# Performance work log

Measured on AMD Instinct MI355X. Metric: run time of the kernel, lower is better.

The kernel has to match this reference:

```python
import jax, jax.numpy as jnp
import numpy as np

N, IN_DIM, OUT_DIM = 8192, 512, 256
ALPHA = 0.2
NEG_INF = -9e15


def setup_inputs() -> dict:
    key = jax.random.key(0)
    k1, k2, k3, k4 = jax.random.split(key, 4)
    node_features = jax.random.normal(k1, (N, IN_DIM), dtype=jnp.float32)
    adj_matrix = jax.random.randint(k2, (N, N), 0, 2, dtype=jnp.int32)
    # xavier-uniform linear weight [out,in] -> store as [in,out]
    lim_w = float(np.sqrt(6.0 / (IN_DIM + OUT_DIM)))
    W = jax.random.uniform(k3, (IN_DIM, OUT_DIM), dtype=jnp.float32, minval=-lim_w, maxval=lim_w)
    b = jnp.zeros((OUT_DIM,), dtype=jnp.float32)
    # attention Linear(2*out_dim, 1): weight a [2*out_dim], bias scalar
    lim_a = float(np.sqrt(6.0 / (2 * OUT_DIM + 1)))
    a = jax.random.uniform(k4, (2 * OUT_DIM,), dtype=jnp.float32, minval=-lim_a, maxval=lim_a)
    a_bias = jnp.zeros((), dtype=jnp.float32)
    return {"adj_matrix": adj_matrix, "node_features": node_features, "W": W, "b": b, "a": a, "a_bias": a_bias}


def reference(adj_matrix, node_features, W, b, a, a_bias):
    # h = Linear(node_features); dropout is identity in eval mode
    h = node_features @ W + b                     # [N, D]
    # attention(cat(h_i, h_j)) == h_i @ a_l + h_j @ a_r + a_bias
    a_l, a_r = a[:OUT_DIM], a[OUT_DIM:]
    e_l = h @ a_l                                 # [N]
    e_r = h @ a_r                                 # [N]
    e = jax.nn.leaky_relu(e_l[:, None] + e_r[None, :] + a_bias, ALPHA)  # [N, N]
    scores = jnp.where(adj_matrix > 0, e, NEG_INF)
    attention = jax.nn.softmax(scores, axis=1)    # [N, N]
    h_prime = attention @ h                       # [N, D]
    return h_prime
```

## Files before the change

### kernel.cpp

```cpp
#include <hip/hip_runtime.h>

#define N 8192
#define DIN 512
#define DOUT 256
#define ALPHA 0.2f
#define NEG_INF -9.0e15f

typedef __attribute__((ext_vector_type(8))) short bf16x8;
typedef __attribute__((ext_vector_type(4))) float f32x4;
typedef __attribute__((ext_vector_type(4))) int   i32x4;

__device__ __forceinline__ unsigned f2bf_u(float f) {
    unsigned u = __builtin_bit_cast(unsigned, f);
    return (u + 0x7fffu + ((u >> 16) & 1u)) >> 16;
}
__device__ __forceinline__ unsigned pack2bf(float lo, float hi) {
    return f2bf_u(lo) | (f2bf_u(hi) << 16);
}
union U4BF8 { uint4 u; bf16x8 v; };

__device__ __forceinline__ void async_copy16(const ushort* g, ushort* l) {
    __builtin_amdgcn_global_load_lds(
        (const __attribute__((address_space(1))) unsigned*)g,
        (__attribute__((address_space(3))) unsigned*)l, 16, 0, 0);
}

__global__ __launch_bounds__(256) void wb_kernel(const float* __restrict__ W,
                                                 ushort* __restrict__ WB) {
    const int g = blockIdx.x * 256 + threadIdx.x;
    const int c = g & 255, k8 = g >> 8;
    const float* wp = W + (size_t)(k8 * 8) * DOUT + c;
    U4BF8 o;
    o.u.x = pack2bf(wp[0 * DOUT], wp[1 * DOUT]);
    o.u.y = pack2bf(wp[2 * DOUT], wp[3 * DOUT]);
    o.u.z = pack2bf(wp[4 * DOUT], wp[5 * DOUT]);
    o.u.w = pack2bf(wp[6 * DOUT], wp[7 * DOUT]);
    *(uint4*)(WB + (size_t)g * 8) = o.u;
}

__global__ __launch_bounds__(256) void h_kernel(
        const float* __restrict__ X, const ushort* __restrict__ WB,
        const float* __restrict__ bvec, const float* __restrict__ a,
        ushort* __restrict__ hB, float* __restrict__ el, float* __restrict__ er)
{
    __shared__ float red[4][64][65];
    __shared__ float elr[2][4][16];
    const int t = threadIdx.x;
    const int w = t >> 6, l = t & 63, q = l >> 4, n = l & 15;
    const int i0 = blockIdx.x * 16;
    f32x4 acc[16];
    #pragma unroll
    for (int ct = 0; ct < 16; ++ct) acc[ct] = (f32x4){0.f, 0.f, 0.f, 0.f};
    const float* xp = X + (size_t)(i0 + n) * DIN + q * 8;

    #pragma unroll
    for (int ks = 0; ks < 4; ++ks) {
        const int k0 = w * 128 + ks * 32;
        const float4 x0 = *(const float4*)(xp + k0);
        const float4 x1 = *(const float4*)(xp + k0 + 4);
        U4BF8 pa;
        pa.u.x = pack2bf(x0.x, x0.y); pa.u.y = pack2bf(x0.z, x0.w);
        pa.u.z = pack2bf(x1.x, x1.y); pa.u.w = pack2bf(x1.z, x1.w);
        const ushort* wbp = WB + ((k0 >> 3) + q) * 2048 + n * 8;
        bf16x8 bfr[16];
        #pragma unroll
        for (int ct = 0; ct < 16; ++ct) bfr[ct] = *(const bf16x8*)(wbp + ct * 128);
        #pragma unroll
        for (int ct = 0; ct < 16; ++ct)
            acc[ct] = __builtin_amdgcn_mfma_f32_16x16x32_bf16(pa.v, bfr[ct], acc[ct], 0, 0, 0);
    }
    #pragma unroll
    for (int ct = 0; ct < 16; ++ct)
        #pragma unroll
        for (int r = 0; r < 4; ++r) red[w][l][ct * 4 + r] = acc[ct][r];
    __syncthreads();

    float pl[4] = {0.f, 0.f, 0.f, 0.f}, pr[4] = {0.f, 0.f, 0.f, 0.f};
    const int hbase = (blockIdx.x * 2 + (q >> 1)) * 2048 + n * 8 + (q & 1) * 4;
    #pragma unroll
    for (int c2 = 0; c2 < 4; ++c2) {
        const int ct = w * 4 + c2;
        const float bb = bvec[ct * 16 + n];
        const float al = a[ct * 16 + n];
        const float ar = a[DOUT + ct * 16 + n];
        float v[4];
        #pragma unroll
        for (int r = 0; r < 4; ++r) {
            v[r] = red[0][l][ct * 4 + r] + red[1][l][ct * 4 + r]
                 + red[2][l][ct * 4 + r] + red[3][l][ct * 4 + r] + bb;
            pl[r] += v[r] * al;
            pr[r] += v[r] * ar;
        }
        ushort4 hp;
        hp.x = (ushort)f2bf_u(v[0]); hp.y = (ushort)f2bf_u(v[1]);
        hp.z = (ushort)f2bf_u(v[2]); hp.w = (ushort)f2bf_u(v[3]);
        *(ushort4*)&hB[hbase + ct * 128] = hp;
    }
    #pragma unroll
    for (int r = 0; r < 4; ++r) {
        #pragma unroll
        for (int off = 1; off < 16; off <<= 1) {
            pl[r] += __shfl_xor(pl[r], off);
            pr[r] += __shfl_xor(pr[r], off);
        }
    }
    if (n == 0) {
        #pragma unroll
        for (int r = 0; r < 4; ++r) {
            elr[0][w][q * 4 + r] = pl[r];
            elr[1][w][q * 4 + r] = pr[r];
        }
    }
    __syncthreads();
    if (t < 16) {
        el[i0 + t] = elr[0][0][t] + elr[0][1][t] + elr[0][2][t] + elr[0][3][t];
        er[i0 + t] = elr[1][0][t] + elr[1][1][t] + elr[1][2][t] + elr[1][3][t];
    }
}

__global__ __launch_bounds__(512, 1) void attn_kernel(
        const int* __restrict__ adj, const float* __restrict__ el,
        const float* __restrict__ er, const float* __restrict__ ab,
        const ushort* __restrict__ hB, float* __restrict__ pout,
        float* __restrict__ plsum)
{
    __shared__ ushort stage[2][32768];
    __shared__ float ers[2048];
    const int t = threadIdx.x;
    const int w = t >> 6, l = t & 63, q = l >> 4, n = l & 15;
    const int rb = blockIdx.x >> 2, jq = blockIdx.x & 3;
    const int j0 = jq * 2048;
    const int row = rb * 128 + w * 16 + n;
    const float elm = el[row] + ab[0];
    const int* alp = adj + (size_t)row * N + j0 + q * 8;

    f32x4 acc[16];
    #pragma unroll
    for (int ct = 0; ct < 16; ++ct) acc[ct] = (f32x4){0.f, 0.f, 0.f, 0.f};
    float lsum = 0.f;

    *(float4*)&ers[t * 4] = *(const float4*)&er[j0 + t * 4];
    i32x4 a[8];
    #pragma unroll
    for (int kg = 0; kg < 4; ++kg) {
        a[2 * kg]     = __builtin_nontemporal_load((const i32x4*)(alp + kg * 32));
        a[2 * kg + 1] = __builtin_nontemporal_load((const i32x4*)(alp + kg * 32 + 4));
    }
    {
        const ushort* g = hB + (size_t)j0 * 256 + t * 8;
        ushort* lb = &stage[0][t * 8];
        #pragma unroll
        for (int i = 0; i < 8; ++i) async_copy16(g + i * 4096, lb + i * 4096);
    }

    for (int s = 0; s < 16; ++s) {
        __syncthreads();
        if (s < 15) {
            const ushort* g = hB + (size_t)(j0 + (s + 1) * 128) * 256 + t * 8;
            ushort* lb = &stage[(s + 1) & 1][t * 8];
            #pragma unroll
            for (int i = 0; i < 8; ++i) async_copy16(g + i * 4096, lb + i * 4096);
        }
        U4BF8 pa[4];
        #pragma unroll
        for (int kg = 0; kg < 4; ++kg) {
            const float4 e0 = *(const float4*)&ers[s * 128 + kg * 32 + q * 8];
            const float4 e1 = *(const float4*)&ers[s * 128 + kg * 32 + q * 8 + 4];
            const i32x4 a0 = a[2 * kg], a1 = a[2 * kg + 1];
            float v, p0, p1, p2, p3, p4, p5, p6, p7;
            v = elm + e0.x; v = fmaxf(v, ALPHA * v); p0 = __expf(a0.x > 0 ? v : NEG_INF);
            v = elm + e0.y; v = fmaxf(v, ALPHA * v); p1 = __expf(a0.y > 0 ? v : NEG_INF);
            v = elm + e0.z; v = fmaxf(v, ALPHA * v); p2 = __expf(a0.z > 0 ? v : NEG_INF);
            v = elm + e0.w; v = fmaxf(v, ALPHA * v); p3 = __expf(a0.w > 0 ? v : NEG_INF);
            v = elm + e1.x; v = fmaxf(v, ALPHA * v); p4 = __expf(a1.x > 0 ? v : NEG_INF);
            v = elm + e1.y; v = fmaxf(v, ALPHA * v); p5 = __expf(a1.y > 0 ? v : NEG_INF);
            v = elm + e1.z; v = fmaxf(v, ALPHA * v); p6 = __expf(a1.z > 0 ? v : NEG_INF);
            v = elm + e1.w; v = fmaxf(v, ALPHA * v); p7 = __expf(a1.w > 0 ? v : NEG_INF);
            lsum += p0 + p1 + p2 + p3 + p4 + p5 + p6 + p7;
            pa[kg].u.x = pack2bf(p0, p1); pa[kg].u.y = pack2bf(p2, p3);
            pa[kg].u.z = pack2bf(p4, p5); pa[kg].u.w = pack2bf(p6, p7);
        }
        if (s < 15) {
            const int* ap = alp + (s + 1) * 128;
            #pragma unroll
            for (int kg = 0; kg < 4; ++kg) {
                a[2 * kg]     = __builtin_nontemporal_load((const i32x4*)(ap + kg * 32));
                a[2 * kg + 1] = __builtin_nontemporal_load((const i32x4*)(ap + kg * 32 + 4));
            }
        }
        #pragma unroll
        for (int kg = 0; kg < 4; ++kg) {
            const ushort* sb = &stage[s & 1][(kg * 4 + q) * 2048 + n * 8];
            #pragma unroll
            for (int ct = 0; ct < 16; ++ct) {
                const bf16x8 bf = *(const bf16x8*)(sb + ct * 128);
                acc[ct] = __builtin_amdgcn_mfma_f32_16x16x32_bf16(pa[kg].v, bf, acc[ct], 0, 0, 0);
            }
        }
    }

    lsum += __shfl_xor(lsum, 16);
    lsum += __shfl_xor(lsum, 32);
    if (l < 16) plsum[(size_t)jq * N + row] = lsum;

    float* pb = pout + ((size_t)jq * N + rb * 128 + w * 16 + q * 4) * 256 + n;
    #pragma unroll
    for (int ct = 0; ct < 16; ++ct)
        #pragma unroll
        for (int r = 0; r < 4; ++r)
            __builtin_nontemporal_store(acc[ct][r], pb + (size_t)r * 256 + ct * 16);
}

__global__ __launch_bounds__(256) void combine_kernel(
        const float* __restrict__ pout, const float* __restrict__ plsum,
        float* __restrict__ out)
{
    const int t = threadIdx.x;
    const int row = blockIdx.x * 4 + (t >> 6);
    const int c = (t & 63) * 4;
    const size_t idx = (size_t)row * 256 + c;
    const size_t qs = (size_t)N * 256;
    float4 v0 = *(const float4*)&pout[idx];
    float4 v1 = *(const float4*)&pout[idx + qs];
    float4 v2 = *(const float4*)&pout[idx + 2 * qs];
    float4 v3 = *(const float4*)&pout[idx + 3 * qs];
    const float li = 1.0f / (plsum[row] + plsum[N + row]
                           + plsum[2 * N + row] + plsum[3 * N + row]);
    float4 o;
    o.x = (v0.x + v1.x + v2.x + v3.x) * li;
    o.y = (v0.y + v1.y + v2.y + v3.y) * li;
    o.z = (v0.z + v1.z + v2.z + v3.z) * li;
    o.w = (v0.w + v1.w + v2.w + v3.w) * li;
    *(float4*)&out[idx] = o;
}

extern "C" void kernel_launch(void* const* d_in, const int* in_sizes, int n_in,
                              void* d_out, int out_size, void* d_ws, size_t ws_size,
                              hipStream_t stream) {
    const int*   adj = (const int*)  d_in[0];
    const float* X   = (const float*)d_in[1];
    const float* W   = (const float*)d_in[2];
    const float* b   = (const float*)d_in[3];
    const float* a   = (const float*)d_in[4];
    const float* ab  = (const float*)d_in[5];
    float* out = (float*)d_out;

    ushort* hB    = (ushort*)d_ws;
    ushort* WB    = hB + (size_t)N * DOUT;
    float*  el    = (float*)(WB + (size_t)DIN * DOUT);
    float*  er    = el + N;
    float*  plsum = er + N;
    float*  pout  = plsum + 4 * N;

    wb_kernel<<<dim3(64), dim3(256), 0, stream>>>(W, WB);
    h_kernel<<<dim3(N / 16), dim3(256), 0, stream>>>(X, WB, b, a, hB, el, er);
    attn_kernel<<<dim3(256), dim3(512), 0, stream>>>(adj, el, er, ab, hB, pout, plsum);
    combine_kernel<<<dim3(N / 4), dim3(256), 0, stream>>>(pout, plsum, out);
}
```

Before: 418.8 us.

## Split attention key range into eight chunks with smaller tiles for occupancy

The attention kernel now splits the key dimension into 8 chunks instead of 4. It launches 512 blocks, halves the LDS staging and per-step tile, and raises the launch-bounds occupancy hint from 1 to 4 blocks. Adjacency loads switch from nontemporal to regular loads, and the combine kernel now reduces 8 partial outputs and 8 partial sums. The goal is more resident waves per CU to hide memory and exp latency. In exchange it writes and re-reads twice as much partial output, and the tighter register budget may force the 64-float accumulators to spill.

```diff
diff --git a/kernel.cpp b/kernel.cpp
--- a/kernel.cpp
+++ b/kernel.cpp
@@ -118,18 +118,34 @@
     }
 }
 
-__global__ __launch_bounds__(512, 1) void attn_kernel(
+#define EXP8(ELM, E0, E1, M0, M1, PA, LS)                                          \
+    {                                                                              \
+        float v, p0, p1, p2, p3, p4, p5, p6, p7;                                   \
+        v = ELM + E0.x; v = fmaxf(v, ALPHA * v); p0 = __expf(M0.x > 0 ? v : NEG_INF); \
+        v = ELM + E0.y; v = fmaxf(v, ALPHA * v); p1 = __expf(M0.y > 0 ? v : NEG_INF); \
+        v = ELM + E0.z; v = fmaxf(v, ALPHA * v); p2 = __expf(M0.z > 0 ? v : NEG_INF); \
+        v = ELM + E0.w; v = fmaxf(v, ALPHA * v); p3 = __expf(M0.w > 0 ? v : NEG_INF); \
+        v = ELM + E1.x; v = fmaxf(v, ALPHA * v); p4 = __expf(M1.x > 0 ? v : NEG_INF); \
+        v = ELM + E1.y; v = fmaxf(v, ALPHA * v); p5 = __expf(M1.y > 0 ? v : NEG_INF); \
+        v = ELM + E1.z; v = fmaxf(v, ALPHA * v); p6 = __expf(M1.z > 0 ? v : NEG_INF); \
+        v = ELM + E1.w; v = fmaxf(v, ALPHA * v); p7 = __expf(M1.w > 0 ? v : NEG_INF); \
+        LS += p0 + p1 + p2 + p3 + p4 + p5 + p6 + p7;                               \
+        PA.u.x = pack2bf(p0, p1); PA.u.y = pack2bf(p2, p3);                        \
+        PA.u.z = pack2bf(p4, p5); PA.u.w = pack2bf(p6, p7);                        \
+    }
+
+__global__ __launch_bounds__(512, 4) void attn_kernel(
         const int* __restrict__ adj, const float* __restrict__ el,
         const float* __restrict__ er, const float* __restrict__ ab,
         const ushort* __restrict__ hB, float* __restrict__ pout,
         float* __restrict__ plsum)
 {
-    __shared__ ushort stage[2][32768];
-    __shared__ float ers[2048];
+    __shared__ ushort stage[2][16384];
+    __shared__ float ers[1024];
     const int t = threadIdx.x;
     const int w = t >> 6, l = t & 63, q = l >> 4, n = l & 15;
-    const int rb = blockIdx.x >> 2, jq = blockIdx.x & 3;
-    const int j0 = jq * 2048;
+    const int rb = blockIdx.x >> 3, je = blockIdx.x & 7;
+    const int j0 = je * 1024;
     const int row = rb * 128 + w * 16 + n;
     const float elm = el[row] + ab[0];
     const int* alp = adj + (size_t)row * N + j0 + q * 8;
@@ -139,57 +155,45 @@
     for (int ct = 0; ct < 16; ++ct) acc[ct] = (f32x4){0.f, 0.f, 0.f, 0.f};
     float lsum = 0.f;
 
-    *(float4*)&ers[t * 4] = *(const float4*)&er[j0 + t * 4];
-    i32x4 a[8];
-    #pragma unroll
-    for (int kg = 0; kg < 4; ++kg) {
-        a[2 * kg]     = __builtin_nontemporal_load((const i32x4*)(alp + kg * 32));
-        a[2 * kg + 1] = __builtin_nontemporal_load((const i32x4*)(alp + kg * 32 + 4));
+    if (t < 256) *(float4*)&ers[t * 4] = *(const float4*)&er[j0 + t * 4];
+    i32x4 a[4];
+    #pragma unroll
+    for (int kg = 0; kg < 2; ++kg) {
+        a[2 * kg]     = *(const i32x4*)(alp + kg * 32);
+        a[2 * kg + 1] = *(const i32x4*)(alp + kg * 32 + 4);
     }
     {
         const ushort* g = hB + (size_t)j0 * 256 + t * 8;
         ushort* lb = &stage[0][t * 8];
         #pragma unroll
-        for (int i = 0; i < 8; ++i) async_copy16(g + i * 4096, lb + i * 4096);
+        for (int i = 0; i < 4; ++i) async_copy16(g + i * 4096, lb + i * 4096);
     }
 
     for (int s = 0; s < 16; ++s) {
         __syncthreads();
         if (s < 15) {
-            const ushort* g = hB + (size_t)(j0 + (s + 1) * 128) * 256 + t * 8;
+            const ushort* g = hB + (size_t)(j0 + (s + 1) * 64) * 256 + t * 8;
             ushort* lb = &stage[(s + 1) & 1][t * 8];
             #pragma unroll
-            for (int i = 0; i < 8; ++i) async_copy16(g + i * 4096, lb + i * 4096);
-        }
-        U4BF8 pa[4];
-        #pragma unroll
-        for (int kg = 0; kg < 4; ++kg) {
-            const float4 e0 = *(const float4*)&ers[s * 128 + kg * 32 + q * 8];
-            const float4 e1 = *(const float4*)&ers[s * 128 + kg * 32 + q * 8 + 4];
-            const i32x4 a0 = a[2 * kg], a1 = a[2 * kg + 1];
-            float v, p0, p1, p2, p3, p4, p5, p6, p7;
-            v = elm + e0.x; v = fmaxf(v, ALPHA * v); p0 = __expf(a0.x > 0 ? v : NEG_INF);
-            v = elm + e0.y; v = fmaxf(v, ALPHA * v); p1 = __expf(a0.y > 0 ? v : NEG_INF);
-            v = elm + e0.z; v = fmaxf(v, ALPHA * v); p2 = __expf(a0.z > 0 ? v : NEG_INF);
-            v = elm + e0.w; v = fmaxf(v, ALPHA * v); p3 = __expf(a0.w > 0 ? v : NEG_INF);
-            v = elm + e1.x; v = fmaxf(v, ALPHA * v); p4 = __expf(a1.x > 0 ? v : NEG_INF);
-            v = elm + e1.y; v = fmaxf(v, ALPHA * v); p5 = __expf(a1.y > 0 ? v : NEG_INF);
-            v = elm + e1.z; v = fmaxf(v, ALPHA * v); p6 = __expf(a1.z > 0 ? v : NEG_INF);
-            v = elm + e1.w; v = fmaxf(v, ALPHA * v); p7 = __expf(a1.w > 0 ? v : NEG_INF);
-            lsum += p0 + p1 + p2 + p3 + p4 + p5 + p6 + p7;
-            pa[kg].u.x = pack2bf(p0, p1); pa[kg].u.y = pack2bf(p2, p3);
-            pa[kg].u.z = pack2bf(p4, p5); pa[kg].u.w = pack2bf(p6, p7);
+            for (int i = 0; i < 4; ++i) async_copy16(g + i * 4096, lb + i * 4096);
+        }
+        U4BF8 pa[2];
+        #pragma unroll
+        for (int kg = 0; kg < 2; ++kg) {
+            const float4 e0 = *(const float4*)&ers[s * 64 + kg * 32 + q * 8];
+            const float4 e1 = *(const float4*)&ers[s * 64 + kg * 32 + q * 8 + 4];
+            EXP8(elm, e0, e1, a[2 * kg], a[2 * kg + 1], pa[kg], lsum);
         }
         if (s < 15) {
-            const int* ap = alp + (s + 1) * 128;
+            const int* ap = alp + (s + 1) * 64;
             #pragma unroll
-            for (int kg = 0; kg < 4; ++kg) {
-                a[2 * kg]     = __builtin_nontemporal_load((const i32x4*)(ap + kg * 32));
-                a[2 * kg + 1] = __builtin_nontemporal_load((const i32x4*)(ap + kg * 32 + 4));
+            for (int kg = 0; kg < 2; ++kg) {
+                a[2 * kg]     = *(const i32x4*)(ap + kg * 32);
+                a[2 * kg + 1] = *(const i32x4*)(ap + kg * 32 + 4);
             }
         }
         #pragma unroll
-        for (int kg = 0; kg < 4; ++kg) {
+        for (int kg = 0; kg < 2; ++kg) {
             const ushort* sb = &stage[s & 1][(kg * 4 + q) * 2048 + n * 8];
             #pragma unroll
             for (int ct = 0; ct < 16; ++ct) {
@@ -201,9 +205,9 @@
 
     lsum += __shfl_xor(lsum, 16);
     lsum += __shfl_xor(lsum, 32);
-    if (l < 16) plsum[(size_t)jq * N + row] = lsum;
-
-    float* pb = pout + ((size_t)jq * N + rb * 128 + w * 16 + q * 4) * 256 + n;
+    if (l < 16) plsum[(size_t)je * N + row] = lsum;
+
+    float* pb = pout + ((size_t)je * N + rb * 128 + w * 16 + q * 4) * 256 + n;
     #pragma unroll
     for (int ct = 0; ct < 16; ++ct)
         #pragma unroll
@@ -220,17 +224,17 @@
     const int c = (t & 63) * 4;
     const size_t idx = (size_t)row * 256 + c;
     const size_t qs = (size_t)N * 256;
-    float4 v0 = *(const float4*)&pout[idx];
-    float4 v1 = *(const float4*)&pout[idx + qs];
-    float4 v2 = *(const float4*)&pout[idx + 2 * qs];
-    float4 v3 = *(const float4*)&pout[idx + 3 * qs];
-    const float li = 1.0f / (plsum[row] + plsum[N + row]
-                           + plsum[2 * N + row] + plsum[3 * N + row]);
+    float4 acc = *(const float4*)&pout[idx];
+    float ls = plsum[row];
+    #pragma unroll
+    for (int k = 1; k < 8; ++k) {
+        const float4 v = *(const float4*)&pout[idx + k * qs];
+        acc.x += v.x; acc.y += v.y; acc.z += v.z; acc.w += v.w;
+        ls += plsum[k * N + row];
+    }
+    const float li = 1.0f / ls;
     float4 o;
-    o.x = (v0.x + v1.x + v2.x + v3.x) * li;
-    o.y = (v0.y + v1.y + v2.y + v3.y) * li;
-    o.z = (v0.z + v1.z + v2.z + v3.z) * li;
-    o.w = (v0.w + v1.w + v2.w + v3.w) * li;
+    o.x = acc.x * li; o.y = acc.y * li; o.z = acc.z * li; o.w = acc.w * li;
     *(float4*)&out[idx] = o;
 }
 
@@ -250,10 +254,10 @@
     float*  el    = (float*)(WB + (size_t)DIN * DOUT);
     float*  er    = el + N;
     float*  plsum = er + N;
-    float*  pout  = plsum + 4 * N;
+    float*  pout  = plsum + 8 * N;
 
     wb_kernel<<<dim3(64), dim3(256), 0, stream>>>(W, WB);
     h_kernel<<<dim3(N / 16), dim3(256), 0, stream>>>(X, WB, b, a, hB, el, er);
-    attn_kernel<<<dim3(256), dim3(512), 0, stream>>>(adj, el, er, ab, hB, pout, plsum);
+    attn_kernel<<<dim3(512), dim3(512), 0, stream>>>(adj, el, er, ab, hB, pout, plsum);
     combine_kernel<<<dim3(N / 4), dim3(256), 0, stream>>>(pout, plsum, out);
 }
```

New measurement: 441.6 us. 5.5% more time.

## Drop LDS staging of h in attention kernel, read B fragments directly from global

Applied to the files above, without the earlier changes.

The attention kernel no longer double-buffers h tiles into LDS with async global-to-LDS copies. Each wave now loads its bf16 B fragments straight from global memory, which relies on hB already being laid out in fragment order and on L2 caching. Blocks shrink from 512 to 256 threads (64 rows per block, 512 blocks, up to 4 blocks per CU) and the k-step shrinks to 64 columns. This removes the LDS footprint and the per-step barriers to allow more occupancy, but every wave now re-reads h from cache instead of sharing one LDS copy per block.

```diff
diff --git a/kernel.cpp b/kernel.cpp
--- a/kernel.cpp
+++ b/kernel.cpp
@@ -18,12 +18,6 @@
     return f2bf_u(lo) | (f2bf_u(hi) << 16);
 }
 union U4BF8 { uint4 u; bf16x8 v; };
-
-__device__ __forceinline__ void async_copy16(const ushort* g, ushort* l) {
-    __builtin_amdgcn_global_load_lds(
-        (const __attribute__((address_space(1))) unsigned*)g,
-        (__attribute__((address_space(3))) unsigned*)l, 16, 0, 0);
-}
 
 __global__ __launch_bounds__(256) void wb_kernel(const float* __restrict__ W,
                                                  ushort* __restrict__ WB) {
@@ -118,19 +112,34 @@
     }
 }
 
-__global__ __launch_bounds__(512, 1) void attn_kernel(
+#define EXP8(ELM, E0, E1, M0, M1, PA, LS)                                          \
+    {                                                                              \
+        float v, p0, p1, p2, p3, p4, p5, p6, p7;                                   \
+        v = ELM + E0.x; v = fmaxf(v, ALPHA * v); p0 = __expf(M0.x > 0 ? v : NEG_INF); \
+        v = ELM + E0.y; v = fmaxf(v, ALPHA * v); p1 = __expf(M0.y > 0 ? v : NEG_INF); \
+        v = ELM + E0.z; v = fmaxf(v, ALPHA * v); p2 = __expf(M0.z > 0 ? v : NEG_INF); \
+        v = ELM + E0.w; v = fmaxf(v, ALPHA * v); p3 = __expf(M0.w > 0 ? v : NEG_INF); \
+        v = ELM + E1.x; v = fmaxf(v, ALPHA * v); p4 = __expf(M1.x > 0 ? v : NEG_INF); \
+        v = ELM + E1.y; v = fmaxf(v, ALPHA * v); p5 = __expf(M1.y > 0 ? v : NEG_INF); \
+        v = ELM + E1.z; v = fmaxf(v, ALPHA * v); p6 = __expf(M1.z > 0 ? v : NEG_INF); \
+        v = ELM + E1.w; v = fmaxf(v, ALPHA * v); p7 = __expf(M1.w > 0 ? v : NEG_INF); \
+        LS += p0 + p1 + p2 + p3 + p4 + p5 + p6 + p7;                               \
+        PA.u.x = pack2bf(p0, p1); PA.u.y = pack2bf(p2, p3);                        \
+        PA.u.z = pack2bf(p4, p5); PA.u.w = pack2bf(p6, p7);                        \
+    }
+
+__global__ __launch_bounds__(256, 4) void attn_kernel(
         const int* __restrict__ adj, const float* __restrict__ el,
         const float* __restrict__ er, const float* __restrict__ ab,
         const ushort* __restrict__ hB, float* __restrict__ pout,
         float* __restrict__ plsum)
 {
-    __shared__ ushort stage[2][32768];
     __shared__ float ers[2048];
     const int t = threadIdx.x;
     const int w = t >> 6, l = t & 63, q = l >> 4, n = l & 15;
     const int rb = blockIdx.x >> 2, jq = blockIdx.x & 3;
     const int j0 = jq * 2048;
-    const int row = rb * 128 + w * 16 + n;
+    const int row = rb * 64 + w * 16 + n;
     const float elm = el[row] + ab[0];
     const int* alp = adj + (size_t)row * N + j0 + q * 8;
 
@@ -139,63 +148,43 @@
     for (int ct = 0; ct < 16; ++ct) acc[ct] = (f32x4){0.f, 0.f, 0.f, 0.f};
     float lsum = 0.f;
 
-    *(float4*)&ers[t * 4] = *(const float4*)&er[j0 + t * 4];
-    i32x4 a[8];
-    #pragma unroll
-    for (int kg = 0; kg < 4; ++kg) {
-        a[2 * kg]     = __builtin_nontemporal_load((const i32x4*)(alp + kg * 32));
-        a[2 * kg + 1] = __builtin_nontemporal_load((const i32x4*)(alp + kg * 32 + 4));
-    }
-    {
-        const ushort* g = hB + (size_t)j0 * 256 + t * 8;
-        ushort* lb = &stage[0][t * 8];
-        #pragma unroll
-        for (int i = 0; i < 8; ++i) async_copy16(g + i * 4096, lb + i * 4096);
-    }
-
-    for (int s = 0; s < 16; ++s) {
-        __syncthreads();
-        if (s < 15) {
-            const ushort* g = hB + (size_t)(j0 + (s + 1) * 128) * 256 + t * 8;
-            ushort* lb = &stage[(s + 1) & 1][t * 8];
-            #pragma unroll
-            for (int i = 0; i < 8; ++i) async_copy16(g + i * 4096, lb + i * 4096);
-        }
-        U4BF8 pa[4];
-        #pragma unroll
-        for (int kg = 0; kg < 4; ++kg) {
-            const float4 e0 = *(const float4*)&ers[s * 128 + kg * 32 + q * 8];
-            const float4 e1 = *(const float4*)&ers[s * 128 + kg * 32 + q * 8 + 4];
-            const i32x4 a0 = a[2 * kg], a1 = a[2 * kg + 1];
-            float v, p0, p1, p2, p3, p4, p5, p6, p7;
-            v = elm + e0.x; v = fmaxf(v, ALPHA * v); p0 = __expf(a0.x > 0 ? v : NEG_INF);
-            v = elm + e0.y; v = fmaxf(v, ALPHA * v); p1 = __expf(a0.y > 0 ? v : NEG_INF);
-            v = elm + e0.z; v = fmaxf(v, ALPHA * v); p2 = __expf(a0.z > 0 ? v : NEG_INF);
-            v = elm + e0.w; v = fmaxf(v, ALPHA * v); p3 = __expf(a0.w > 0 ? v : NEG_INF);
-            v = elm + e1.x; v = fmaxf(v, ALPHA * v); p4 = __expf(a1.x > 0 ? v : NEG_INF);
-            v = elm + e1.y; v = fmaxf(v, ALPHA * v); p5 = __expf(a1.y > 0 ? v : NEG_INF);
-            v = elm + e1.z; v = fmaxf(v, ALPHA * v); p6 = __expf(a1.z > 0 ? v : NEG_INF);
-            v = elm + e1.w; v = fmaxf(v, ALPHA * v); p7 = __expf(a1.w > 0 ? v : NEG_INF);
-            lsum += p0 + p1 + p2 + p3 + p4 + p5 + p6 + p7;
-            pa[kg].u.x = pack2bf(p0, p1); pa[kg].u.y = pack2bf(p2, p3);
-            pa[kg].u.z = pack2bf(p4, p5); pa[kg].u.w = pack2bf(p6, p7);
-        }
-        if (s < 15) {
-            const int* ap = alp + (s + 1) * 128;
-            #pragma unroll
-            for (int kg = 0; kg < 4; ++kg) {
-                a[2 * kg]     = __builtin_nontemporal_load((const i32x4*)(ap + kg * 32));
-                a[2 * kg + 1] = __builtin_nontemporal_load((const i32x4*)(ap + kg * 32 + 4));
-            }
-        }
-        #pragma unroll
-        for (int kg = 0; kg < 4; ++kg) {
-            const ushort* sb = &stage[s & 1][(kg * 4 + q) * 2048 + n * 8];
-            #pragma unroll
-            for (int ct = 0; ct < 16; ++ct) {
-                const bf16x8 bf = *(const bf16x8*)(sb + ct * 128);
-                acc[ct] = __builtin_amdgcn_mfma_f32_16x16x32_bf16(pa[kg].v, bf, acc[ct], 0, 0, 0);
-            }
+    *(float4*)&ers[t * 8]     = *(const float4*)&er[j0 + t * 8];
+    *(float4*)&ers[t * 8 + 4] = *(const float4*)&er[j0 + t * 8 + 4];
+    __syncthreads();
+
+    i32x4 am0 = __builtin_nontemporal_load((const i32x4*)(alp + 0));
+    i32x4 am1 = __builtin_nontemporal_load((const i32x4*)(alp + 4));
+    i32x4 am2 = __builtin_nontemporal_load((const i32x4*)(alp + 32));
+    i32x4 am3 = __builtin_nontemporal_load((const i32x4*)(alp + 36));
+
+    for (int s = 0; s < 32; ++s) {
+        U4BF8 pa0, pa1;
+        {
+            const float4 e00 = *(const float4*)&ers[s * 64 + q * 8];
+            const float4 e01 = *(const float4*)&ers[s * 64 + q * 8 + 4];
+            EXP8(elm, e00, e01, am0, am1, pa0, lsum);
+            const float4 e10 = *(const float4*)&ers[s * 64 + 32 + q * 8];
+            const float4 e11 = *(const float4*)&ers[s * 64 + 32 + q * 8 + 4];
+            EXP8(elm, e10, e11, am2, am3, pa1, lsum);
+        }
+        if (s < 31) {
+            const int* ap = alp + (s + 1) * 64;
+            am0 = __builtin_nontemporal_load((const i32x4*)(ap + 0));
+            am1 = __builtin_nontemporal_load((const i32x4*)(ap + 4));
+            am2 = __builtin_nontemporal_load((const i32x4*)(ap + 32));
+            am3 = __builtin_nontemporal_load((const i32x4*)(ap + 36));
+        }
+        const ushort* bp0 = hB + (size_t)(jq * 256 + s * 8 + q) * 2048 + n * 8;
+        const ushort* bp1 = bp0 + (size_t)4 * 2048;
+        #pragma unroll
+        for (int ct = 0; ct < 16; ++ct) {
+            const bf16x8 bf = *(const bf16x8*)(bp0 + ct * 128);
+            acc[ct] = __builtin_amdgcn_mfma_f32_16x16x32_bf16(pa0.v, bf, acc[ct], 0, 0, 0);
+        }
+        #pragma unroll
+        for (int ct = 0; ct < 16; ++ct) {
+            const bf16x8 bf = *(const bf16x8*)(bp1 + ct * 128);
+            acc[ct] = __builtin_amdgcn_mfma_f32_16x16x32_bf16(pa1.v, bf, acc[ct], 0, 0, 0);
         }
     }
 
@@ -203,7 +192,7 @@
     lsum += __shfl_xor(lsum, 32);
     if (l < 16) plsum[(size_t)jq * N + row] = lsum;
 
-    float* pb = pout + ((size_t)jq * N + rb * 128 + w * 16 + q * 4) * 256 + n;
+    float* pb = pout + ((size_t)jq * N + rb * 64 + w * 16 + q * 4) * 256 + n;
     #pragma unroll
     for (int ct = 0; ct < 16; ++ct)
         #pragma unroll
@@ -254,6 +243,6 @@
 
     wb_kernel<<<dim3(64), dim3(256), 0, stream>>>(W, WB);
     h_kernel<<<dim3(N / 16), dim3(256), 0, stream>>>(X, WB, b, a, hB, el, er);
-    attn_kernel<<<dim3(256), dim3(512), 0, stream>>>(adj, el, er, ab, hB, pout, plsum);
+    attn_kernel<<<dim3(512), dim3(256), 0, stream>>>(adj, el, er, ab, hB, pout, plsum);
     combine_kernel<<<dim3(N / 4), dim3(256), 0, stream>>>(pout, plsum, out);
 }
```

Result: slower. 692.7 us (+65.4%).
